# Kernel tuning notes

Measured on AMD Instinct MI355X. Metric: run time of the kernel, lower is better.

## Reference

```python
import jax, jax.numpy as jnp
import numpy as np


def setup_inputs() -> dict:
    key = jax.random.key(0)
    ks = jax.random.split(key, 10)
    B, T, H, V = 32, 512, 1024, 32000
    s = 1.0 / np.sqrt(H)  # pytorch LSTM init scale
    tgt = jax.random.randint(ks[0], (B, T), 0, V, dtype=jnp.int64)
    emb_table = jax.random.normal(ks[1], (V, H), dtype=jnp.float32)
    emb_table = emb_table.at[0].set(0.0)  # padding_idx=0 row is zero
    return {
        "tgt": tgt,
        "h0": jax.random.normal(ks[2], (1, B, H), dtype=jnp.float32),
        "c0": jax.random.normal(ks[3], (1, B, H), dtype=jnp.float32),
        "encoder_outputs": jax.random.normal(ks[4], (B, 64, H), dtype=jnp.float32),
        "src_lengths": jax.random.randint(ks[5], (B,), 1, 64, dtype=jnp.int64),
        "emb_table": emb_table,
        "W_ih": jax.random.uniform(ks[6], (4 * H, H), jnp.float32, -s, s),
        "W_hh": jax.random.uniform(ks[7], (4 * H, H), jnp.float32, -s, s),
        "b_ih": jax.random.uniform(ks[8], (4 * H,), jnp.float32, -s, s),
        "b_hh": jax.random.uniform(ks[9], (4 * H,), jnp.float32, -s, s),
    }


def _lstm_scan(emb, h0, c0, W_ih, W_hh, b_ih, b_hh):
    # emb: [B, T, H]; h0/c0: [B, H]. PyTorch gate order: i, f, g, o.
    H = h0.shape[-1]
    # precompute input-to-hidden projection for all steps at once: [T, B, 4H]
    x_proj = jnp.einsum('bth,gh->tbg', emb, W_ih) + b_ih + b_hh

    def step(carry, xp_t):
        h, c = carry
        gates = xp_t + h @ W_hh.T  # [B, 4H]
        i = jax.nn.sigmoid(gates[:, 0 * H:1 * H])
        f = jax.nn.sigmoid(gates[:, 1 * H:2 * H])
        g = jnp.tanh(gates[:, 2 * H:3 * H])
        o = jax.nn.sigmoid(gates[:, 3 * H:4 * H])
        c = f * c + i * g
        h = o * jnp.tanh(c)
        return (h, c), h

    (hT, cT), hs = jax.lax.scan(step, (h0, c0), x_proj)
    return jnp.swapaxes(hs, 0, 1), hT, cT  # [B, T, H], [B, H], [B, H]


def reference(tgt, h0, c0, encoder_outputs, src_lengths, emb_table, W_ih, W_hh, b_ih, b_hh):
    # dec_state has num_layers=1 so the reshape_state branch is skipped.
    # Dropout is identity (eval mode). encoder_outputs/src_lengths are unused
    # (attn is never called in the original forward).
    x = tgt[:, :-1] if tgt.shape[1] > 1 else tgt
    emb = emb_table[x]  # [B, T-1, H]
    res, hT, cT = _lstm_scan(emb, h0[0], c0[0], W_ih, W_hh, b_ih, b_hh)
    return res, (hT[None], cT[None])
```

## Files before the change

### kernel.cpp

```cpp
#include <hip/hip_runtime.h>


typedef __bf16 bf16;
typedef __bf16 bf16x4 __attribute__((ext_vector_type(4)));
typedef __bf16 bf16x8 __attribute__((ext_vector_type(8)));
typedef float f32x4 __attribute__((ext_vector_type(4)));
typedef float f32x16 __attribute__((ext_vector_type(16)));

#define M_TOT 16352
#define RES_STRIDE 523264
#define HT_OFF 16744448
#define CT_OFF 16777216

__device__ __forceinline__ uint4 load_coherent16(const void* p) {
    uint4 r;
    asm volatile("global_load_dwordx4 %0, %1, off sc0 sc1" : "=v"(r) : "v"(p));
    return r;
}
__device__ __forceinline__ unsigned int load_coherent4(const void* p) {
    unsigned int r;
    asm volatile("global_load_dword %0, %1, off sc0 sc1\n\ts_waitcnt vmcnt(0)"
                 : "=v"(r) : "v"(p) : "memory");
    return r;
}
__device__ __forceinline__ void store_coherent2(void* p, unsigned int v) {
    asm volatile("global_store_short %0, %1, off sc0 sc1" :: "v"(p), "v"(v) : "memory");
}
__device__ __forceinline__ void store_coherent4(void* p, unsigned int v) {
    asm volatile("global_store_dword %0, %1, off sc0 sc1" :: "v"(p), "v"(v) : "memory");
}
__device__ __forceinline__ void wait_vm0() {
    asm volatile("s_waitcnt vmcnt(0)" ::: "memory");
}

__global__ void cvt_kernel(const float* __restrict__ src, bf16* __restrict__ dst, int n4) {
    int i = blockIdx.x * blockDim.x + threadIdx.x;
    if (i < n4) {
        float4 v = ((const float4*)src)[i];
        bf16x4 o;
        o[0] = (bf16)v.x; o[1] = (bf16)v.y; o[2] = (bf16)v.z; o[3] = (bf16)v.w;
        ((bf16x4*)dst)[i] = o;
    }
}

__global__ void init_state(const float* __restrict__ h0, bf16* __restrict__ hx) {
    int i = blockIdx.x * blockDim.x + threadIdx.x;
    if (i < 32768) {
        int b = i >> 10, col = i & 1023;
        int blk = col >> 4, c = col & 15;
        hx[blk * 512 + b * 16 + c] = (bf16)h0[i];
    }
}

__global__ __launch_bounds__(256) void gemm_xproj(
    const int* __restrict__ tgt, const bf16* __restrict__ emb,
    const bf16* __restrict__ wih, const float* __restrict__ bih,
    const float* __restrict__ bhh, bf16* __restrict__ P)
{
    __shared__ bf16 As[128 * 72];
    __shared__ bf16 Bs[128 * 72];
    __shared__ int tok[128];

    const int tid  = threadIdx.x;
    const int lane = tid & 63;
    const int wave = tid >> 6;
    const int wm = wave & 1, wn = wave >> 1;
    const int tileM = blockIdx.y * 128;
    const int tileN = blockIdx.x * 128;

    if (tid < 128) {
        int m = tileM + tid;
        int token = 0;
        if (m < M_TOT) {
            int t = m >> 5, b = m & 31;
            token = tgt[b * 512 + t];
            if ((unsigned)token >= 32000u) token = 0;
        }
        tok[tid] = token;
    }
    __syncthreads();

    f32x4 acc[4][4] = {};

    for (int k0 = 0; k0 < 1024; k0 += 64) {
        #pragma unroll
        for (int i = 0; i < 4; ++i) {
            int chunk = i * 256 + tid;
            int row = chunk >> 3;
            int kc  = (chunk & 7) * 8;
            const bf16* srcA = emb + (long)tok[row] * 1024 + k0 + kc;
            *(uint4*)&As[row * 72 + kc] = *(const uint4*)srcA;
            const bf16* srcB = wih + (long)(tileN + row) * 1024 + k0 + kc;
            *(uint4*)&Bs[row * 72 + kc] = *(const uint4*)srcB;
        }
        __syncthreads();
        #pragma unroll
        for (int kk = 0; kk < 64; kk += 32) {
            bf16x8 a[4], b[4];
            #pragma unroll
            for (int f = 0; f < 4; ++f) {
                a[f] = *(const bf16x8*)&As[(wm * 64 + f * 16 + (lane & 15)) * 72 + kk + (lane >> 4) * 8];
                b[f] = *(const bf16x8*)&Bs[(wn * 64 + f * 16 + (lane & 15)) * 72 + kk + (lane >> 4) * 8];
            }
            #pragma unroll
            for (int mf = 0; mf < 4; ++mf)
                #pragma unroll
                for (int nf = 0; nf < 4; ++nf)
                    acc[mf][nf] = __builtin_amdgcn_mfma_f32_16x16x32_bf16(a[mf], b[nf], acc[mf][nf], 0, 0, 0);
        }
        __syncthreads();
    }

    float bias[4];
    #pragma unroll
    for (int nf = 0; nf < 4; ++nf) {
        int j = tileN + wn * 64 + nf * 16 + (lane & 15);
        bias[nf] = bih[j] + bhh[j];
    }
    #pragma unroll
    for (int mf = 0; mf < 4; ++mf) {
        int mBase = tileM + wm * 64 + mf * 16 + ((lane >> 4) * 4);
        #pragma unroll
        for (int r = 0; r < 4; ++r) {
            int m = mBase + r;
            if (m < M_TOT) {
                int t = m >> 5, bb = m & 31;
                #pragma unroll
                for (int nf = 0; nf < 4; ++nf) {
                    int j = tileN + wn * 64 + nf * 16 + (lane & 15);
                    int gate = j >> 10, jc = j & 1023;
                    int pblk = jc >> 4, pc = jc & 15;
                    P[((long)(t * 64 + pblk)) * 2048 + gate * 512 + bb * 16 + pc]
                        = (bf16)(acc[mf][nf][r] + bias[nf]);
                }
            }
        }
    }
}

__global__ __launch_bounds__(512, 1) void lstm_persist(
    const bf16* __restrict__ P, const bf16* __restrict__ whh,
    const float* __restrict__ c0, float* __restrict__ out,
    bf16* __restrict__ hxA, bf16* __restrict__ hxB,
    unsigned int* __restrict__ flags)
{
    __shared__ bf16  hs[32 * 1024];
    __shared__ float gs[4 * 64 * 33];
    __shared__ bf16  ps[2048];

    const int tid  = threadIdx.x;
    const int lane = tid & 63;
    const int wave = tid >> 6;
    const int blk  = blockIdx.x;

    const int tp    = wave & 1;
    const int ks    = wave >> 1;
    const int cc    = lane & 31;
    const int khalf = lane >> 5;
    const int o     = tp * 32 + cc;

    bf16x8 wreg[16];
    {
        const int gate = tp * 2 + (cc >> 4);
        const int wRow = gate * 1024 + blk * 16 + (cc & 15);
        const bf16* wbase = whh + (long)wRow * 1024 + ks * 256 + khalf * 8;
        #pragma unroll
        for (int i = 0; i < 16; ++i) wreg[i] = *(const bf16x8*)(wbase + i * 16);
    }

    const int eb = tid >> 4;
    const int ec = tid & 15;
    const int hcol = blk * 16 + ec;
    float cReg = c0[eb * 1024 + hcol];

    const int m = lane & 31;

    for (int t = 0; t < 511; ++t) {
        const bf16* hin  = (t & 1) ? hxB : hxA;
        bf16*       hout = (t & 1) ? hxA : hxB;

        uint4 v[8];
        #pragma unroll
        for (int j = 0; j < 8; ++j) {
            int q = j * 512 + tid;
            v[j] = load_coherent16((const char*)hin + q * 16);
        }
        uint2 pv = *(const uint2*)((const char*)P + ((long)(t * 64 + blk)) * 4096 + tid * 8);
        wait_vm0();
        #pragma unroll
        for (int j = 0; j < 8; ++j) {
            int q = j * 512 + tid;
            int sb  = q >> 6;
            int idx = q & 63;
            int b   = idx >> 1;
            int hf  = idx & 1;
            int ch  = sb * 2 + hf;
            *(uint4*)&hs[b * 1024 + ((ch ^ (b & 7)) << 3)] = v[j];
        }
        *(uint2*)&ps[tid * 4] = pv;
        __syncthreads();

        f32x16 acc = {};
        #pragma unroll
        for (int i = 0; i < 16; ++i) {
            int ch = ks * 32 + i * 2 + khalf;
            bf16x8 a = *(const bf16x8*)&hs[m * 1024 + ((ch ^ (m & 7)) << 3)];
            acc = __builtin_amdgcn_mfma_f32_32x32x16_bf16(a, wreg[i], acc, 0, 0, 0);
        }

        #pragma unroll
        for (int r = 0; r < 16; ++r) {
            int b = (r & 3) + 8 * (r >> 2) + 4 * khalf;
            gs[(ks * 64 + o) * 33 + b] = acc[r];
        }
        __syncthreads();

        float g4[4];
        #pragma unroll
        for (int g = 0; g < 4; ++g) {
            int oo = (g >> 1) * 32 + (g & 1) * 16 + ec;
            float s = gs[(0 * 64 + oo) * 33 + eb] + gs[(1 * 64 + oo) * 33 + eb]
                    + gs[(2 * 64 + oo) * 33 + eb] + gs[(3 * 64 + oo) * 33 + eb];
            g4[g] = s + (float)ps[g * 512 + eb * 16 + ec];
        }
        float ig = 1.f / (1.f + __expf(-g4[0]));
        float fg = 1.f / (1.f + __expf(-g4[1]));
        float gg = tanhf(g4[2]);
        float og = 1.f / (1.f + __expf(-g4[3]));
        cReg = fg * cReg + ig * gg;
        float hnew = og * tanhf(cReg);

        if (t < 510) {
            bf16 hb = (bf16)hnew;
            unsigned int bits = (unsigned int)__builtin_bit_cast(unsigned short, hb);
            store_coherent2((char*)hout + (blk * 512 + tid) * 2, bits);
            wait_vm0();
            __syncthreads();
            if (tid == 0) store_coherent4(flags + blk * 32, (unsigned)(t + 1));
            out[(long)eb * RES_STRIDE + (long)t * 1024 + hcol] = hnew;
            if (tid < 64) {
                const unsigned int* fp = flags + tid * 32;
                unsigned int target = (unsigned)(t + 1);
                while (true) {
                    unsigned int fv = load_coherent4(fp);
                    if (__all((int)(fv >= target))) break;
                }
            }
            __syncthreads();
        } else {
            out[(long)eb * RES_STRIDE + (long)t * 1024 + hcol] = hnew;
            out[HT_OFF + eb * 1024 + hcol] = hnew;
            out[CT_OFF + eb * 1024 + hcol] = cReg;
        }
    }
}

extern "C" void kernel_launch(void* const* d_in, const int* in_sizes, int n_in,
                              void* d_out, int out_size, void* d_ws, size_t ws_size,
                              hipStream_t stream) {
    const int*   tgt  = (const int*)d_in[0];
    const float* h0   = (const float*)d_in[1];
    const float* c0   = (const float*)d_in[2];
    const float* embT = (const float*)d_in[5];
    const float* wih  = (const float*)d_in[6];
    const float* whh  = (const float*)d_in[7];
    const float* bih  = (const float*)d_in[8];
    const float* bhh  = (const float*)d_in[9];
    float* out = (float*)d_out;

    char* ws = (char*)d_ws;
    bf16*  P    = (bf16*)(ws);
    bf16*  embB = (bf16*)(ws + 133955584);
    bf16*  wihB = (bf16*)(ws + 199491584);
    bf16*  whhB = (bf16*)(ws + 207880192);
    bf16*  hxA  = (bf16*)(ws + 216268800);
    bf16*  hxB  = (bf16*)(ws + 216334336);
    unsigned int* flags = (unsigned int*)(ws + 216399872);

    hipMemsetAsync(flags, 0, 64 * 32 * 4, stream);

    cvt_kernel<<<32000, 256, 0, stream>>>(embT, embB, 32768000 / 4);
    cvt_kernel<<<4096, 256, 0, stream>>>(wih, wihB, 4194304 / 4);
    cvt_kernel<<<4096, 256, 0, stream>>>(whh, whhB, 4194304 / 4);
    init_state<<<128, 256, 0, stream>>>(h0, hxA);

    dim3 g(32, 128);
    gemm_xproj<<<g, 256, 0, stream>>>(tgt, embB, wihB, bih, bhh, P);

    lstm_persist<<<64, 512, 0, stream>>>(P, whhB, c0, out, hxA, hxB, flags);
}
```

Baseline: 2.339 ms.

## Replace flag barrier with tagged hidden-state packets and prefetch next step

Drops the per-step global flag barrier in the persistent LSTM kernel. Each hidden-state packet now carries the step index as a tag, and consumers poll on the data itself until every tag matches. The next step's hidden state and x-projection are issued right after the store, so their latency overlaps the output write. Sigmoid and tanh are replaced with rcp/exp approximations. The cost is doubled hidden-state traffic from the tag padding and some accuracy risk from the fast transcendentals.

```diff
diff --git a/kernel.cpp b/kernel.cpp
--- a/kernel.cpp
+++ b/kernel.cpp
@@ -6,31 +6,37 @@
 typedef __bf16 bf16x8 __attribute__((ext_vector_type(8)));
 typedef float f32x4 __attribute__((ext_vector_type(4)));
 typedef float f32x16 __attribute__((ext_vector_type(16)));
+typedef unsigned int u32x2 __attribute__((ext_vector_type(2)));
+typedef unsigned int u32x4 __attribute__((ext_vector_type(4)));
 
 #define M_TOT 16352
 #define RES_STRIDE 523264
 #define HT_OFF 16744448
 #define CT_OFF 16777216
 
-__device__ __forceinline__ uint4 load_coherent16(const void* p) {
-    uint4 r;
-    asm volatile("global_load_dwordx4 %0, %1, off sc0 sc1" : "=v"(r) : "v"(p));
+__device__ __forceinline__ u32x4 load_cg_sv(unsigned voff, const void* sbase) {
+    u32x4 r;
+    asm volatile("global_load_dwordx4 %0, %1, %2 sc0 sc1"
+                 : "=v"(r) : "v"(voff), "s"(sbase));
     return r;
 }
-__device__ __forceinline__ unsigned int load_coherent4(const void* p) {
-    unsigned int r;
-    asm volatile("global_load_dword %0, %1, off sc0 sc1\n\ts_waitcnt vmcnt(0)"
-                 : "=v"(r) : "v"(p) : "memory");
-    return r;
-}
-__device__ __forceinline__ void store_coherent2(void* p, unsigned int v) {
-    asm volatile("global_store_short %0, %1, off sc0 sc1" :: "v"(p), "v"(v) : "memory");
-}
-__device__ __forceinline__ void store_coherent4(void* p, unsigned int v) {
-    asm volatile("global_store_dword %0, %1, off sc0 sc1" :: "v"(p), "v"(v) : "memory");
+__device__ __forceinline__ void store_coherent16(void* p, u32x4 v) {
+    asm volatile("global_store_dwordx4 %0, %1, off sc0 sc1" :: "v"(p), "v"(v) : "memory");
 }
 __device__ __forceinline__ void wait_vm0() {
     asm volatile("s_waitcnt vmcnt(0)" ::: "memory");
+}
+__device__ __forceinline__ unsigned pack2bf(float a, float b) {
+    unsigned ua = (unsigned)__builtin_bit_cast(unsigned short, (bf16)a);
+    unsigned ub = (unsigned)__builtin_bit_cast(unsigned short, (bf16)b);
+    return ua | (ub << 16);
+}
+__device__ __forceinline__ float fsig(float x) {
+    return __builtin_amdgcn_rcpf(1.f + __expf(-x));
+}
+__device__ __forceinline__ float ftanh(float x) {
+    float e = __expf(2.f * x);
+    return 1.f - 2.f * __builtin_amdgcn_rcpf(e + 1.f);
 }
 
 __global__ void cvt_kernel(const float* __restrict__ src, bf16* __restrict__ dst, int n4) {
@@ -43,12 +49,16 @@
     }
 }
 
-__global__ void init_state(const float* __restrict__ h0, bf16* __restrict__ hx) {
-    int i = blockIdx.x * blockDim.x + threadIdx.x;
-    if (i < 32768) {
-        int b = i >> 10, col = i & 1023;
-        int blk = col >> 4, c = col & 15;
-        hx[blk * 512 + b * 16 + c] = (bf16)h0[i];
+__global__ void init_state(const float* __restrict__ h0, u32x4* __restrict__ hxA) {
+    int n = blockIdx.x * blockDim.x + threadIdx.x;
+    if (n < 8192) {
+        int blk = n >> 7, b = (n >> 2) & 31, e4 = n & 3;
+        const float* src = h0 + b * 1024 + blk * 16 + e4 * 4;
+        u32x4 v;
+        v.x = pack2bf(src[0], src[1]);
+        v.y = pack2bf(src[2], src[3]);
+        v.z = 0u; v.w = 0u;
+        hxA[n] = v;
     }
 }
 
@@ -141,12 +151,11 @@
 __global__ __launch_bounds__(512, 1) void lstm_persist(
     const bf16* __restrict__ P, const bf16* __restrict__ whh,
     const float* __restrict__ c0, float* __restrict__ out,
-    bf16* __restrict__ hxA, bf16* __restrict__ hxB,
-    unsigned int* __restrict__ flags)
+    u32x4* __restrict__ hxA, u32x4* __restrict__ hxB)
 {
     __shared__ bf16  hs[32 * 1024];
     __shared__ float gs[4 * 64 * 33];
-    __shared__ bf16  ps[2048];
+    __shared__ bf16  ps[2][2048];
 
     const int tid  = threadIdx.x;
     const int lane = tid & 63;
@@ -175,29 +184,38 @@
 
     const int m = lane & 31;
 
+    const unsigned voff = (unsigned)(tid << 4);
+    const int srow = (tid >> 2) & 31;
+    const int chb  = ((tid >> 7) << 1) | ((tid & 3) >> 1);
+    const int s7   = srow & 7;
+    char* hsb = (char*)hs + srow * 2048 + (tid & 1) * 8;
+
+    uint2 pv = *(const uint2*)((const char*)P + ((long)blk) * 4096 + tid * 8);
+    u32x4 u[16];
+    #pragma unroll
+    for (int j = 0; j < 16; ++j)
+        u[j] = load_cg_sv(voff, (const char*)hxA + j * 8192);
+
     for (int t = 0; t < 511; ++t) {
-        const bf16* hin  = (t & 1) ? hxB : hxA;
-        bf16*       hout = (t & 1) ? hxA : hxB;
-
-        uint4 v[8];
-        #pragma unroll
-        for (int j = 0; j < 8; ++j) {
-            int q = j * 512 + tid;
-            v[j] = load_coherent16((const char*)hin + q * 16);
-        }
-        uint2 pv = *(const uint2*)((const char*)P + ((long)(t * 64 + blk)) * 4096 + tid * 8);
-        wait_vm0();
-        #pragma unroll
-        for (int j = 0; j < 8; ++j) {
-            int q = j * 512 + tid;
-            int sb  = q >> 6;
-            int idx = q & 63;
-            int b   = idx >> 1;
-            int hf  = idx & 1;
-            int ch  = sb * 2 + hf;
-            *(uint4*)&hs[b * 1024 + ((ch ^ (b & 7)) << 3)] = v[j];
-        }
-        *(uint2*)&ps[tid * 4] = pv;
+        const char* hb = (const char*)((t & 1) ? hxB : hxA);
+        const unsigned exptag = (unsigned)t;
+
+        for (;;) {
+            wait_vm0();
+            __builtin_amdgcn_sched_barrier(0);
+            unsigned bad = 0;
+            #pragma unroll
+            for (int j = 0; j < 16; ++j) bad |= (u[j].z ^ exptag);
+            if (bad == 0) break;
+            #pragma unroll
+            for (int j = 0; j < 16; ++j)
+                u[j] = load_cg_sv(voff, hb + j * 8192);
+        }
+
+        #pragma unroll
+        for (int j = 0; j < 16; ++j)
+            *(uint2*)(hsb + (((j * 8 + chb) ^ s7) << 4)) = make_uint2(u[j].x, u[j].y);
+        *(uint2*)&ps[t & 1][tid * 4] = pv;
         __syncthreads();
 
         f32x16 acc = {};
@@ -221,32 +239,31 @@
             int oo = (g >> 1) * 32 + (g & 1) * 16 + ec;
             float s = gs[(0 * 64 + oo) * 33 + eb] + gs[(1 * 64 + oo) * 33 + eb]
                     + gs[(2 * 64 + oo) * 33 + eb] + gs[(3 * 64 + oo) * 33 + eb];
-            g4[g] = s + (float)ps[g * 512 + eb * 16 + ec];
-        }
-        float ig = 1.f / (1.f + __expf(-g4[0]));
-        float fg = 1.f / (1.f + __expf(-g4[1]));
-        float gg = tanhf(g4[2]);
-        float og = 1.f / (1.f + __expf(-g4[3]));
+            g4[g] = s + (float)ps[t & 1][g * 512 + eb * 16 + ec];
+        }
+        float ig = fsig(g4[0]);
+        float fg = fsig(g4[1]);
+        float gg = ftanh(g4[2]);
+        float og = fsig(g4[3]);
         cReg = fg * cReg + ig * gg;
-        float hnew = og * tanhf(cReg);
+        float hnew = og * ftanh(cReg);
 
         if (t < 510) {
-            bf16 hb = (bf16)hnew;
-            unsigned int bits = (unsigned int)__builtin_bit_cast(unsigned short, hb);
-            store_coherent2((char*)hout + (blk * 512 + tid) * 2, bits);
-            wait_vm0();
-            __syncthreads();
-            if (tid == 0) store_coherent4(flags + blk * 32, (unsigned)(t + 1));
+            unsigned w = (unsigned)__builtin_bit_cast(unsigned short, (bf16)hnew);
+            unsigned p1  = (unsigned)__builtin_amdgcn_mov_dpp((int)w,   0xB1, 0xF, 0xF, true);
+            unsigned w01 = (tid & 1) ? (p1 | (w << 16)) : (w | (p1 << 16));
+            unsigned w23 = (unsigned)__builtin_amdgcn_mov_dpp((int)w01, 0x4E, 0xF, 0xF, true);
+            char* hob = (char*)((t & 1) ? hxA : hxB);
+            if ((tid & 3) == 0) {
+                u32x4 st;
+                st.x = w01; st.y = w23; st.z = (unsigned)(t + 1); st.w = st.z;
+                store_coherent16(hob + blk * 2048 + (tid >> 2) * 16, st);
+            }
+            pv = *(const uint2*)((const char*)P + ((long)((t + 1) * 64 + blk)) * 4096 + tid * 8);
+            #pragma unroll
+            for (int j = 0; j < 16; ++j)
+                u[j] = load_cg_sv(voff, (const char*)hob + j * 8192);
             out[(long)eb * RES_STRIDE + (long)t * 1024 + hcol] = hnew;
-            if (tid < 64) {
-                const unsigned int* fp = flags + tid * 32;
-                unsigned int target = (unsigned)(t + 1);
-                while (true) {
-                    unsigned int fv = load_coherent4(fp);
-                    if (__all((int)(fv >= target))) break;
-                }
-            }
-            __syncthreads();
         } else {
             out[(long)eb * RES_STRIDE + (long)t * 1024 + hcol] = hnew;
             out[HT_OFF + eb * 1024 + hcol] = hnew;
@@ -269,23 +286,22 @@
     float* out = (float*)d_out;
 
     char* ws = (char*)d_ws;
-    bf16*  P    = (bf16*)(ws);
+    bf16*  Pb   = (bf16*)(ws);
     bf16*  embB = (bf16*)(ws + 133955584);
     bf16*  wihB = (bf16*)(ws + 199491584);
     bf16*  whhB = (bf16*)(ws + 207880192);
-    bf16*  hxA  = (bf16*)(ws + 216268800);
-    bf16*  hxB  = (bf16*)(ws + 216334336);
-    unsigned int* flags = (unsigned int*)(ws + 216399872);
-
-    hipMemsetAsync(flags, 0, 64 * 32 * 4, stream);
+    u32x4* hxA  = (u32x4*)(ws + 216268800);
+    u32x4* hxB  = (u32x4*)(ws + 216399872);
+
+    (void)hipMemsetAsync(hxB, 0xFF, 131072, stream);
 
     cvt_kernel<<<32000, 256, 0, stream>>>(embT, embB, 32768000 / 4);
     cvt_kernel<<<4096, 256, 0, stream>>>(wih, wihB, 4194304 / 4);
     cvt_kernel<<<4096, 256, 0, stream>>>(whh, whhB, 4194304 / 4);
-    init_state<<<128, 256, 0, stream>>>(h0, hxA);
+    init_state<<<32, 256, 0, stream>>>(h0, hxA);
 
     dim3 g(32, 128);
-    gemm_xproj<<<g, 256, 0, stream>>>(tgt, embB, wihB, bih, bhh, P);
-
-    lstm_persist<<<64, 512, 0, stream>>>(P, whhB, c0, out, hxA, hxB, flags);
-}
+    gemm_xproj<<<g, 256, 0, stream>>>(tgt, embB, wihB, bih, bhh, Pb);
+
+    lstm_persist<<<64, 512, 0, stream>>>(Pb, whhB, c0, out, hxA, hxB);
+}
```

Result: slower. 2.780 ms (+18.8%).

## Replace global barrier with per-wave flag polling and prefetch next-step projections

Applied to the files above, without the earlier changes.

The all-block spin barrier after each timestep is removed. Each wave now polls the producer flags for the 8 hidden-state chunks it needs and loads each chunk as soon as its flag is ready, so consumers can start while other blocks are still writing. Flags are packed contiguously, the next step's input projection is prefetched after the flag store, and sigmoid/tanh switch to rcp-based fast approximations. The cost is finer-grained polling traffic, a possible memory-ordering risk between the flag store and the data loads, and slightly less accurate activations.

```diff
diff --git a/kernel.cpp b/kernel.cpp
--- a/kernel.cpp
+++ b/kernel.cpp
@@ -6,21 +6,21 @@
 typedef __bf16 bf16x8 __attribute__((ext_vector_type(8)));
 typedef float f32x4 __attribute__((ext_vector_type(4)));
 typedef float f32x16 __attribute__((ext_vector_type(16)));
+typedef unsigned int u32x4 __attribute__((ext_vector_type(4)));
 
 #define M_TOT 16352
 #define RES_STRIDE 523264
 #define HT_OFF 16744448
 #define CT_OFF 16777216
 
-__device__ __forceinline__ uint4 load_coherent16(const void* p) {
-    uint4 r;
+__device__ __forceinline__ u32x4 load_coherent16(const void* p) {
+    u32x4 r;
     asm volatile("global_load_dwordx4 %0, %1, off sc0 sc1" : "=v"(r) : "v"(p));
     return r;
 }
-__device__ __forceinline__ unsigned int load_coherent4(const void* p) {
-    unsigned int r;
-    asm volatile("global_load_dword %0, %1, off sc0 sc1\n\ts_waitcnt vmcnt(0)"
-                 : "=v"(r) : "v"(p) : "memory");
+__device__ __forceinline__ unsigned load_cg4(const void* p) {
+    unsigned r;
+    asm volatile("global_load_dword %0, %1, off sc0 sc1" : "=v"(r) : "v"(p));
     return r;
 }
 __device__ __forceinline__ void store_coherent2(void* p, unsigned int v) {
@@ -31,6 +31,13 @@
 }
 __device__ __forceinline__ void wait_vm0() {
     asm volatile("s_waitcnt vmcnt(0)" ::: "memory");
+}
+__device__ __forceinline__ float fsig(float x) {
+    return __builtin_amdgcn_rcpf(1.f + __expf(-x));
+}
+__device__ __forceinline__ float ftanh(float x) {
+    float e = __expf(2.f * x);
+    return 1.f - 2.f * __builtin_amdgcn_rcpf(e + 1.f);
 }
 
 __global__ void cvt_kernel(const float* __restrict__ src, bf16* __restrict__ dst, int n4) {
@@ -175,18 +182,33 @@
 
     const int m = lane & 31;
 
+    const unsigned ownbit = (wave == (blk & 7)) ? (1u << (blk >> 3)) : 0u;
+
+    uint2 pv = *(const uint2*)((const char*)P + ((long)blk) * 4096 + tid * 8);
+
     for (int t = 0; t < 511; ++t) {
-        const bf16* hin  = (t & 1) ? hxB : hxA;
-        bf16*       hout = (t & 1) ? hxA : hxB;
-
-        uint4 v[8];
-        #pragma unroll
-        for (int j = 0; j < 8; ++j) {
-            int q = j * 512 + tid;
-            v[j] = load_coherent16((const char*)hin + q * 16);
-        }
-        uint2 pv = *(const uint2*)((const char*)P + ((long)(t * 64 + blk)) * 4096 + tid * 8);
+        const char* hin = (const char*)((t & 1) ? hxB : hxA);
+        const unsigned tgtf = (unsigned)t;
+
+        u32x4 v[8];
+        unsigned pend = 0xFFu;
+        unsigned newly = ownbit;
+        for (;;) {
+            #pragma unroll
+            for (int j = 0; j < 8; ++j)
+                if ((newly >> j) & 1)
+                    v[j] = load_coherent16(hin + (j * 512 + tid) * 16);
+            pend &= ~newly;
+            if (pend == 0) break;
+            unsigned f = 0;
+            if (lane < 8) f = load_cg4(flags + (lane * 8 + wave));
+            wait_vm0();
+            __builtin_amdgcn_sched_barrier(0);
+            newly = ((unsigned)__ballot((int)(f >= tgtf)) & 0xFFu) & pend;
+        }
         wait_vm0();
+        __builtin_amdgcn_sched_barrier(0);
+
         #pragma unroll
         for (int j = 0; j < 8; ++j) {
             int q = j * 512 + tid;
@@ -195,7 +217,7 @@
             int b   = idx >> 1;
             int hf  = idx & 1;
             int ch  = sb * 2 + hf;
-            *(uint4*)&hs[b * 1024 + ((ch ^ (b & 7)) << 3)] = v[j];
+            *(u32x4*)&hs[b * 1024 + ((ch ^ (b & 7)) << 3)] = v[j];
         }
         *(uint2*)&ps[tid * 4] = pv;
         __syncthreads();
@@ -223,30 +245,23 @@
                     + gs[(2 * 64 + oo) * 33 + eb] + gs[(3 * 64 + oo) * 33 + eb];
             g4[g] = s + (float)ps[g * 512 + eb * 16 + ec];
         }
-        float ig = 1.f / (1.f + __expf(-g4[0]));
-        float fg = 1.f / (1.f + __expf(-g4[1]));
-        float gg = tanhf(g4[2]);
-        float og = 1.f / (1.f + __expf(-g4[3]));
+        float ig = fsig(g4[0]);
+        float fg = fsig(g4[1]);
+        float gg = ftanh(g4[2]);
+        float og = fsig(g4[3]);
         cReg = fg * cReg + ig * gg;
-        float hnew = og * tanhf(cReg);
+        float hnew = og * ftanh(cReg);
 
         if (t < 510) {
             bf16 hb = (bf16)hnew;
             unsigned int bits = (unsigned int)__builtin_bit_cast(unsigned short, hb);
-            store_coherent2((char*)hout + (blk * 512 + tid) * 2, bits);
+            char* hout = (char*)((t & 1) ? hxA : hxB);
+            store_coherent2(hout + (blk * 512 + tid) * 2, bits);
             wait_vm0();
             __syncthreads();
-            if (tid == 0) store_coherent4(flags + blk * 32, (unsigned)(t + 1));
+            if (tid == 0) store_coherent4(flags + blk, (unsigned)(t + 1));
+            pv = *(const uint2*)((const char*)P + ((long)((t + 1) * 64 + blk)) * 4096 + tid * 8);
             out[(long)eb * RES_STRIDE + (long)t * 1024 + hcol] = hnew;
-            if (tid < 64) {
-                const unsigned int* fp = flags + tid * 32;
-                unsigned int target = (unsigned)(t + 1);
-                while (true) {
-                    unsigned int fv = load_coherent4(fp);
-                    if (__all((int)(fv >= target))) break;
-                }
-            }
-            __syncthreads();
         } else {
             out[(long)eb * RES_STRIDE + (long)t * 1024 + hcol] = hnew;
             out[HT_OFF + eb * 1024 + hcol] = hnew;
@@ -269,7 +284,7 @@
     float* out = (float*)d_out;
 
     char* ws = (char*)d_ws;
-    bf16*  P    = (bf16*)(ws);
+    bf16*  Pb   = (bf16*)(ws);
     bf16*  embB = (bf16*)(ws + 133955584);
     bf16*  wihB = (bf16*)(ws + 199491584);
     bf16*  whhB = (bf16*)(ws + 207880192);
@@ -277,7 +292,7 @@
     bf16*  hxB  = (bf16*)(ws + 216334336);
     unsigned int* flags = (unsigned int*)(ws + 216399872);
 
-    hipMemsetAsync(flags, 0, 64 * 32 * 4, stream);
+    (void)hipMemsetAsync(flags, 0, 64 * 4, stream);
 
     cvt_kernel<<<32000, 256, 0, stream>>>(embT, embB, 32768000 / 4);
     cvt_kernel<<<4096, 256, 0, stream>>>(wih, wihB, 4194304 / 4);
@@ -285,7 +300,7 @@
     init_state<<<128, 256, 0, stream>>>(h0, hxA);
 
     dim3 g(32, 128);
-    gemm_xproj<<<g, 256, 0, stream>>>(tgt, embB, wihB, bih, bhh, P);
-
-    lstm_persist<<<64, 512, 0, stream>>>(P, whhB, c0, out, hxA, hxB, flags);
-}
+    gemm_xproj<<<g, 256, 0, stream>>>(tgt, embB, wihB, bih, bhh, Pb);
+
+    lstm_persist<<<64, 512, 0, stream>>>(Pb, whhB, c0, out, hxA, hxB, flags);
+}
```

Measured after the change: 2.252 ms. 1.04x faster.
